# Optimization experiments

Hardware: AMD Instinct MI355X
Metric: run time of the kernel (lower is better)

Reference implementation:

```python
import jax, jax.numpy as jnp
import numpy as np

B, L, D = 2, 4096, 2048
H = 8
DK = D // H   # head qk dim = 256
DV = D // H   # head v dim = 256
KCONV = 4
BT = 64       # chunk size
EPS = 1e-5


def setup_inputs() -> dict:
    key = jax.random.key(0)
    ks = jax.random.split(key, 10)
    s = 0.02  # xavier-ish init scale (gain 2**-2.5)
    return {
        "hidden_states": jax.random.normal(ks[0], (B, L, D), jnp.float32),
        "Wq": jax.random.normal(ks[1], (D, D), jnp.float32) * s,
        "Wk": jax.random.normal(ks[2], (D, D), jnp.float32) * s,
        "Wv": jax.random.normal(ks[3], (D, D), jnp.float32) * s,
        "Wb": jax.random.normal(ks[4], (H, D), jnp.float32) * s,
        "conv_q": jax.random.normal(ks[5], (D, KCONV), jnp.float32) * 0.5,
        "conv_k": jax.random.normal(ks[6], (D, KCONV), jnp.float32) * 0.5,
        "conv_v": jax.random.normal(ks[7], (D, KCONV), jnp.float32) * 0.5,
        "g_norm": jnp.ones((DV,), jnp.float32),
        "Wo": jax.random.normal(ks[8], (D, D), jnp.float32) * s,
    }


def _causal_conv_silu(x, w):
    # depthwise causal conv1d (ShortConvolution), x: [B,L,C], w: [C,K]; silu activation
    K = w.shape[1]
    xp = jnp.pad(x, ((0, 0), (K - 1, 0), (0, 0)))
    Lx = x.shape[1]
    y = xp[:, 0:Lx, :] * w[:, 0]
    for j in range(1, K):
        y = y + xp[:, j:j + Lx, :] * w[:, j]
    return jax.nn.silu(y)


def _l2norm(x):
    return x * jax.lax.rsqrt(jnp.sum(x * x, -1, keepdims=True) + 1e-6)


def _chunk_delta_rule(q, k, v, beta):
    # q,k: [B,H,L,DK], v: [B,H,L,DV], beta: [B,H,L]
    b, h, Lq, dk = q.shape
    dv = v.shape[-1]
    nc = Lq // BT
    q = q * (dk ** -0.5)
    kb = k * beta[..., None]
    vb = v * beta[..., None]
    ch = lambda x: x.reshape(b, h, nc, BT, x.shape[-1])
    qc, kc, kbc, vbc = ch(q), ch(k), ch(kb), ch(vb)
    tri_s = jnp.tril(jnp.ones((BT, BT), bool), -1)  # strictly lower
    tri = jnp.tril(jnp.ones((BT, BT), bool))        # lower incl diag
    # M = strict_lower(K_beta K^T); T = (I+M)^{-1} via unit-lower triangular solve
    M = jnp.where(tri_s, jnp.einsum('bhntd,bhnsd->bhnts', kbc, kc), 0.0)
    Lmat = jnp.eye(BT, dtype=q.dtype) + M
    W = jax.scipy.linalg.solve_triangular(Lmat, kbc, lower=True, unit_diagonal=True)  # T @ k_beta
    U = jax.scipy.linalg.solve_triangular(Lmat, vbc, lower=True, unit_diagonal=True)  # T @ v_beta

    def step(S, xs):
        q_i, k_i, w_i, u_i = xs  # each [b,h,BT,d]
        attn = jnp.where(tri, jnp.einsum('bhtd,bhsd->bhts', q_i, k_i), 0.0)
        u_new = u_i - jnp.einsum('bhtd,bhdv->bhtv', w_i, S)
        o_i = jnp.einsum('bhtd,bhdv->bhtv', q_i, S) + jnp.einsum('bhts,bhsv->bhtv', attn, u_new)
        S = S + jnp.einsum('bhtd,bhtv->bhdv', k_i, u_new)
        return S, o_i

    mv = lambda x: jnp.moveaxis(x, 2, 0)  # chunk axis to front for scan
    S0 = jnp.zeros((b, h, dk, dv), q.dtype)
    S, o = jax.lax.scan(step, S0, (mv(qc), mv(kc), mv(W), mv(U)))
    o = jnp.moveaxis(o, 0, 2).reshape(b, h, Lq, dv)
    return o, S


def reference(hidden_states, Wq, Wk, Wv, Wb, conv_q, conv_k, conv_v, g_norm, Wo):
    hs = hidden_states
    q = _causal_conv_silu(hs @ Wq.T, conv_q)
    k = _causal_conv_silu(hs @ Wk.T, conv_k)
    v = _causal_conv_silu(hs @ Wv.T, conv_v)
    tohead = lambda x: x.reshape(B, L, H, -1).transpose(0, 2, 1, 3)  # b l (h d) -> b h l d
    q, k, v = tohead(q), tohead(k), tohead(v)
    q, k = _l2norm(q), _l2norm(k)
    beta = jax.nn.sigmoid(hs @ Wb.T).transpose(0, 2, 1)  # [B,H,L]
    o, _ = _chunk_delta_rule(q, k, v, beta)
    o = o.transpose(0, 2, 1, 3)  # [B,L,H,DV]
    o = o * jax.lax.rsqrt(jnp.mean(o * o, -1, keepdims=True) + EPS) * g_norm  # per-head RMSNorm
    return o.reshape(B, L, D) @ Wo.T
```

## Files before the change

### kernel.cpp

```cpp
#include <hip/hip_runtime.h>
#include <stdint.h>

#define TOK    8192
#define LDIM   4096
#define DDIM   2048
#define NBH    16
#define DK     256
#define NCHUNK 64
#define DVS    16

typedef __attribute__((ext_vector_type(8))) short bf16x8;
typedef __attribute__((ext_vector_type(4))) float f32x4;

#define MFMA(a,b,c) __builtin_amdgcn_mfma_f32_16x16x32_bf16((a),(b),(c),0,0,0)

__device__ __forceinline__ unsigned short f2bf(float f){
  union { float f; uint32_t u; } v; v.f = f;
  uint32_t r = v.u + 0x7FFFu + ((v.u >> 16) & 1u);
  return (unsigned short)(r >> 16);
}
__device__ __forceinline__ float bf2f(unsigned short u){
  union { uint32_t u; float f; } v; v.u = ((uint32_t)u) << 16;
  return v.f;
}

typedef __attribute__((address_space(1))) unsigned int as1_u32;
typedef __attribute__((address_space(3))) unsigned int as3_u32;
__device__ __forceinline__ void gload16(const void* g, void* l){
  __builtin_amdgcn_global_load_lds((const as1_u32*)g, (as3_u32*)l, 16, 0, 0);
}

__global__ void k_guard(float* o){ if (threadIdx.x == 0) o[0] = 0.f; }

__global__ __launch_bounds__(256) void k_f2bf(const float* __restrict__ s,
                                              unsigned short* __restrict__ d, int n)
{
  int i = (blockIdx.x*256 + threadIdx.x)*4;
  if (i >= n) return;
  float4 v = *(const float4*)(s + i);
  ushort4 o; o.x=f2bf(v.x); o.y=f2bf(v.y); o.z=f2bf(v.z); o.w=f2bf(v.w);
  *(ushort4*)(d + i) = o;
}

__global__ __launch_bounds__(256) void k_beta(const float* __restrict__ hs,
                                              const float* __restrict__ Wb,
                                              float* __restrict__ beta)
{
  const long t = blockIdx.x;
  const int tid = threadIdx.x;
  float acc[8] = {0,0,0,0,0,0,0,0};
  const float* xr = hs + t*DDIM;
  for (int i = tid; i < DDIM; i += 256){
    float x = xr[i];
    #pragma unroll
    for (int h=0; h<8; h++) acc[h] += x * Wb[h*DDIM + i];
  }
  __shared__ float red[8][4];
  const int w = tid >> 6, lane = tid & 63;
  #pragma unroll
  for (int h=0; h<8; h++){
    float s = acc[h];
    #pragma unroll
    for (int off=32; off; off>>=1) s += __shfl_down(s, off, 64);
    if (lane == 0) red[h][w] = s;
  }
  __syncthreads();
  if (tid < 8){
    float s = red[tid][0]+red[tid][1]+red[tid][2]+red[tid][3];
    float bv = 1.f/(1.f + __expf(-s));
    int b = (int)(t >> 12), l = (int)(t & 4095);
    beta[((long)(b*8 + tid))*LDIM + l] = bv;
  }
}

template <bool F32OUT>
__global__ __launch_bounds__(256,2) void k_gemm_bt(
    const unsigned short* __restrict__ A, const unsigned short* __restrict__ Bw,
    void* __restrict__ Cv, int M, int N, int K)
{
  __shared__ unsigned short As[128*32];
  __shared__ unsigned short Bs[128*32];
  const int tid = threadIdx.x;
  const int w = tid >> 6, l = tid & 63;
  const int lo = l & 15, quad = l >> 4;
  const int wm = w >> 1, wn = w & 1;
  const int gx = gridDim.x;
  int id = blockIdx.y * gx + blockIdx.x;
  const int nwg = gx * gridDim.y;
  if ((nwg & 7) == 0){
    const int q8 = nwg >> 3;
    id = (id & 7) * q8 + (id >> 3);
  }
  const int bx = id % gx, by = id / gx;
  const long tm = (long)by * 128, tn = (long)bx * 128;
  const int slot0 = (w*2+0)*64 + l;
  const int slot1 = (w*2+1)*64 + l;
  const int r0 = slot0 >> 2, c0 = (slot0 & 3) * 8;
  const int r1 = slot1 >> 2, c1 = (slot1 & 3) * 8;
  const unsigned short* pA0 = A  + (tm + r0)*(long)K + c0;
  const unsigned short* pA1 = A  + (tm + r1)*(long)K + c1;
  const unsigned short* pB0 = Bw + (tn + r0)*(long)K + c0;
  const unsigned short* pB1 = Bw + (tn + r1)*(long)K + c1;
  unsigned short* lA0 = &As[slot0*8]; unsigned short* lA1 = &As[slot1*8];
  unsigned short* lB0 = &Bs[slot0*8]; unsigned short* lB1 = &Bs[slot1*8];
  f32x4 acc[4][4] = {};
  for (int k0 = 0; k0 < K; k0 += 32){
    __syncthreads();
    gload16(pA0 + k0, lA0);
    gload16(pA1 + k0, lA1);
    gload16(pB0 + k0, lB0);
    gload16(pB1 + k0, lB1);
    __syncthreads();
    bf16x8 af[4], bg[4];
    #pragma unroll
    for (int i=0;i<4;i++){
      af[i] = *(const bf16x8*)&As[(wm*64 + i*16 + lo)*32 + quad*8];
      bg[i] = *(const bf16x8*)&Bs[(wn*64 + i*16 + lo)*32 + quad*8];
    }
    #pragma unroll
    for (int mt=0; mt<4; mt++)
      #pragma unroll
      for (int nt=0; nt<4; nt++)
        acc[mt][nt] = MFMA(af[mt], bg[nt], acc[mt][nt]);
  }
  #pragma unroll
  for (int mt=0; mt<4; mt++)
    #pragma unroll
    for (int nt=0; nt<4; nt++)
      #pragma unroll
      for (int r=0; r<4; r++){
        long m = tm + wm*64 + mt*16 + quad*4 + r;
        long n = tn + wn*64 + nt*16 + lo;
        if (F32OUT) ((float*)Cv)[m*N + n] = acc[mt][nt][r];
        else ((unsigned short*)Cv)[m*N + n] = f2bf(acc[mt][nt][r]);
      }
}

__global__ __launch_bounds__(256) void k_conv(
  const unsigned short* __restrict__ X, const float* __restrict__ Wc,
  const float* __restrict__ beta,
  unsigned short* __restrict__ O, int mode)
{
  const int lt = blockIdx.x, bh = blockIdx.y;
  const int b = bh >> 3, h = bh & 7;
  const int d = threadIdx.x;
  const int ch = h*256 + d;
  const int l0 = lt*64;
  const unsigned short* xp = X + (long)b*LDIM*DDIM + ch;
  const float4 wv = *(const float4*)(Wc + ch*4);
  float x0=0.f, x1=0.f, x2=0.f;
  if (l0 >= 3){
    x0 = bf2f(xp[(long)(l0-3)*DDIM]);
    x1 = bf2f(xp[(long)(l0-2)*DDIM]);
    x2 = bf2f(xp[(long)(l0-1)*DDIM]);
  }
  float y[64];
  #pragma unroll
  for (int i=0;i<64;i++){
    float x3 = bf2f(xp[(long)(l0+i)*DDIM]);
    float s = x0*wv.x + x1*wv.y + x2*wv.z + x3*wv.w;
    y[i] = s / (1.f + __expf(-s));
    x0 = x1; x1 = x2; x2 = x3;
  }
  unsigned short* op = O + (long)bh*LDIM*DK + d;
  if (mode == 2){
    const float* bet = beta + (long)bh*LDIM + l0;
    #pragma unroll
    for (int i=0;i<64;i++) op[(long)(l0+i)*DK] = f2bf(y[i]*bet[i]);
    return;
  }
  __shared__ float red[64*4];
  __shared__ float scl[64];
  const int wv_i = threadIdx.x >> 6, lane = threadIdx.x & 63;
  #pragma unroll
  for (int i=0;i<64;i++){
    float ss = y[i]*y[i];
    #pragma unroll
    for (int off=32; off; off>>=1) ss += __shfl_down(ss, off, 64);
    if (lane == 0) red[i*4 + wv_i] = ss;
  }
  __syncthreads();
  if (threadIdx.x < 64){
    int i = threadIdx.x;
    float s = red[i*4]+red[i*4+1]+red[i*4+2]+red[i*4+3];
    scl[i] = rsqrtf(s + 1e-6f) * (mode==0 ? 0.0625f : 1.f);
  }
  __syncthreads();
  #pragma unroll
  for (int i=0;i<64;i++) op[(long)(l0+i)*DK] = f2bf(y[i]*scl[i]);
}

__global__ __launch_bounds__(256) void k_transpose(
  const unsigned short* __restrict__ kH, unsigned short* __restrict__ kT)
{
  const int lt = blockIdx.x, dt = blockIdx.y, bh = blockIdx.z;
  __shared__ unsigned short tk[64][72];
  const int tid = threadIdx.x;
  const int rl = tid >> 2, c0 = (tid & 3) * 16;
  const long base = ((long)bh*LDIM + lt*64 + rl)*DK + dt*64 + c0;
  *(bf16x8*)&tk[rl][c0]   = *(const bf16x8*)(kH + base);
  *(bf16x8*)&tk[rl][c0+8] = *(const bf16x8*)(kH + base + 8);
  __syncthreads();
  const int rd = tid >> 2, lc0 = (tid & 3) * 16;
  bf16x8 ok0, ok1;
  #pragma unroll
  for (int j=0;j<16;j++){
    unsigned short kraw = tk[lc0+j][rd];
    if (j < 8) ok0[j] = (short)kraw; else ok1[j-8] = (short)kraw;
  }
  const long ob = (((long)bh*NCHUNK + lt)*DK + dt*64 + rd)*64 + lc0;
  *(bf16x8*)(kT + ob) = ok0; *(bf16x8*)(kT + ob + 8) = ok1;
}

__global__ __launch_bounds__(256) void k_passA(
  const unsigned short* __restrict__ qH, const unsigned short* __restrict__ kH,
  const unsigned short* vbH,
  const unsigned short* __restrict__ kT,
  const float* __restrict__ beta,
  unsigned short* Wout,
  unsigned short* __restrict__ Uout,
  unsigned short* __restrict__ Aout)
{
  const int c = blockIdx.x, bh = blockIdx.y;
  __shared__ unsigned short Nn[64*72];
  __shared__ unsigned short NT[64*72];
  __shared__ unsigned short Pb[64*72];
  __shared__ unsigned short vT[256*72];
  const int tid = threadIdx.x;
  const int w = tid >> 6, l = tid & 63, lo = l & 15, quad = l >> 4;
  const long tokBase = (long)bh*LDIM + c*64;
  const unsigned short* qrow = qH + tokBase*DK;
  const unsigned short* krow = kH + tokBase*DK;
  const float bv = beta[tokBase + w*16 + lo];

  {
    const int r = tid >> 2, cs = (tid & 3) * 64;
    const unsigned short* vrow = vbH + (tokBase + r)*DK + cs;
    bf16x8 vv[8];
    #pragma unroll
    for (int j=0;j<8;j++) vv[j] = *(const bf16x8*)(vrow + j*8);
    #pragma unroll
    for (int j=0;j<8;j++)
      #pragma unroll
      for (int e=0;e<8;e++)
        vT[(cs + j*8 + e)*72 + r] = (unsigned short)vv[j][e];
  }

  f32x4 mAcc[4] = {}; f32x4 aAcc[4] = {};
  #pragma unroll
  for (int ks=0; ks<8; ks++){
    bf16x8 kf[4];
    #pragma unroll
    for (int nt=0; nt<4; nt++)
      kf[nt] = *(const bf16x8*)&krow[(nt*16+lo)*DK + ks*32 + quad*8];
    bf16x8 qf  = *(const bf16x8*)&qrow[(w*16+lo)*DK + ks*32 + quad*8];
    bf16x8 kfw = *(const bf16x8*)&krow[(w*16+lo)*DK + ks*32 + quad*8];
    bf16x8 kbf;
    #pragma unroll
    for (int j=0;j<8;j++) kbf[j] = (short)f2bf(bf2f((unsigned short)kfw[j]) * bv);
    #pragma unroll
    for (int nt=0; nt<4; nt++){
      mAcc[nt] = MFMA(kbf, kf[nt], mAcc[nt]);
      aAcc[nt] = MFMA(qf,  kf[nt], aAcc[nt]);
    }
  }
  unsigned short* Ap = Aout + ((long)bh*NCHUNK + c)*64*64;
  #pragma unroll
  for (int nt=0; nt<4; nt++)
    #pragma unroll
    for (int r=0; r<4; r++){
      int t = w*16 + quad*4 + r, s = nt*16 + lo;
      float mv = (t > s) ? mAcc[nt][r] : 0.f;
      unsigned short mb = f2bf(mv);
      Nn[t*72+s] = mb;
      NT[s*72+t] = mb;
      Pb[t*72+s] = f2bf((t==s ? 1.f : 0.f) - mv);
      Ap[t*64+s] = f2bf((t >= s) ? aAcc[nt][r] : 0.f);
    }
  __syncthreads();

  #pragma unroll 1
  for (int it=0; it<5; it++){
    bf16x8 aN[2], aP[2], bN[2][4];
    #pragma unroll
    for (int ks=0; ks<2; ks++){
      aN[ks] = *(const bf16x8*)&Nn[(w*16+lo)*72 + ks*32 + quad*8];
      aP[ks] = *(const bf16x8*)&Pb[(w*16+lo)*72 + ks*32 + quad*8];
      #pragma unroll
      for (int nt=0; nt<4; nt++)
        bN[ks][nt] = *(const bf16x8*)&NT[(nt*16+lo)*72 + ks*32 + quad*8];
    }
    f32x4 pp[4];
    #pragma unroll
    for (int nt=0; nt<4; nt++)
      #pragma unroll
      for (int r=0; r<4; r++)
        pp[nt][r] = bf2f(Pb[(w*16+quad*4+r)*72 + nt*16+lo]);
    __syncthreads();
    f32x4 sq[4] = {};
    #pragma unroll
    for (int ks=0; ks<2; ks++)
      #pragma unroll
      for (int nt=0; nt<4; nt++)
        sq[nt] = MFMA(aN[ks], bN[ks][nt], sq[nt]);
    #pragma unroll
    for (int nt=0; nt<4; nt++)
      #pragma unroll
      for (int r=0; r<4; r++){
        int t = w*16 + quad*4 + r, s = nt*16 + lo;
        unsigned short vb2 = f2bf(sq[nt][r]);
        Nn[t*72+s] = vb2; NT[s*72+t] = vb2;
      }
    __syncthreads();
    #pragma unroll
    for (int ks=0; ks<2; ks++)
      #pragma unroll
      for (int nt=0; nt<4; nt++){
        bf16x8 b = *(const bf16x8*)&NT[(nt*16+lo)*72 + ks*32 + quad*8];
        pp[nt] = MFMA(aP[ks], b, pp[nt]);
      }
    #pragma unroll
    for (int nt=0; nt<4; nt++)
      #pragma unroll
      for (int r=0; r<4; r++)
        Pb[(w*16+quad*4+r)*72 + nt*16+lo] = f2bf(pp[nt][r]);
    __syncthreads();
  }

  float b8[2][8];
  #pragma unroll
  for (int ks=0; ks<2; ks++)
    #pragma unroll
    for (int e=0; e<8; e++)
      b8[ks][e] = beta[tokBase + ks*32 + quad*8 + e];
  const unsigned short* kTb = kT + ((long)bh*NCHUNK + c)*DK*64;
  unsigned short* Wp = Wout + tokBase*DK;
  unsigned short* Up = Uout + tokBase*DK;
  #pragma unroll 1
  for (int nl=0; nl<4; nl++){
    const int d = (w*4 + nl)*16 + lo;
    f32x4 wa[4] = {}; f32x4 ua[4] = {};
    #pragma unroll
    for (int ks=0; ks<2; ks++){
      bf16x8 braw = *(const bf16x8*)&kTb[(long)d*64 + ks*32 + quad*8];
      bf16x8 bw;
      #pragma unroll
      for (int e=0; e<8; e++) bw[e] = (short)f2bf(bf2f((unsigned short)braw[e]) * b8[ks][e]);
      bf16x8 bu = *(const bf16x8*)&vT[d*72 + ks*32 + quad*8];
      #pragma unroll
      for (int mt=0; mt<4; mt++){
        bf16x8 a = *(const bf16x8*)&Pb[(mt*16+lo)*72 + ks*32 + quad*8];
        wa[mt] = MFMA(a, bw, wa[mt]);
        ua[mt] = MFMA(a, bu, ua[mt]);
      }
    }
    #pragma unroll
    for (int mt=0; mt<4; mt++)
      #pragma unroll
      for (int r=0; r<4; r++){
        int t = mt*16 + quad*4 + r;
        Wp[t*DK + d] = f2bf(wa[mt][r]);
        Up[t*DK + d] = f2bf(ua[mt][r]);
      }
  }
}

__device__ __forceinline__ int sidx(int n, int d){
  return n*256 + (((d>>3) ^ (n&7))<<3) + (d&7);
}
__device__ __forceinline__ int uidx(int n, int t){
  return n*64 + ((((t>>3) ^ (n&7)) & 7)<<3) + (t&7);
}

struct PrefWU {
  bf16x8 wf[8];
  unsigned short uf[4];
};

__device__ __forceinline__ void load_wu(PrefWU& P,
    const unsigned short* __restrict__ Wp, const unsigned short* __restrict__ Up,
    int c, int w, int lo, int quad, int vb)
{
  const unsigned short* Wc = Wp + (long)c*64*DK;
  const unsigned short* Uc = Up + (long)c*64*DK;
  #pragma unroll
  for (int ks=0; ks<8; ks++)
    P.wf[ks] = *(const bf16x8*)&Wc[(w*16+lo)*DK + ks*32 + quad*8];
  const int t0 = w*16 + quad*4;
  #pragma unroll
  for (int r=0; r<4; r++)
    P.uf[r] = Uc[(t0+r)*DK + vb*DVS + lo];
}

__device__ __forceinline__ void scan_chunk(PrefWU& P, int c, int cnext,
  const unsigned short* __restrict__ Wp, const unsigned short* __restrict__ Up,
  const unsigned short* __restrict__ qp, const unsigned short* __restrict__ kTp,
  const unsigned short* __restrict__ Ap, unsigned short* __restrict__ op,
  const unsigned short* __restrict__ Srd, unsigned short* __restrict__ Swr,
  unsigned short* __restrict__ u_l, f32x4 (&S)[4],
  int w, int lo, int quad, int vb)
{
  const unsigned short* qc = qp + (long)c*64*DK;
  const unsigned short* Ac = Ap + (long)c*64*64;
  const unsigned short* kc = kTp + (long)c*DK*64;
  const int t0 = w*16 + quad*4;
  bf16x8 qf[8], af[2];
  #pragma unroll
  for (int ks=0; ks<8; ks++)
    qf[ks] = *(const bf16x8*)&qc[(w*16+lo)*DK + ks*32 + quad*8];
  #pragma unroll
  for (int ks=0; ks<2; ks++)
    af[ks] = *(const bf16x8*)&Ac[(w*16+lo)*64 + ks*32 + quad*8];

  bf16x8 sb[8];
  #pragma unroll
  for (int ks=0; ks<8; ks++)
    sb[ks] = *(const bf16x8*)&Srd[sidx(lo, ks*32+quad*8)];
  f32x4 ua0 = {}, ua1 = {};
  #pragma unroll
  for (int ks=0; ks<4; ks++){
    ua0 = MFMA(P.wf[ks],   sb[ks],   ua0);
    ua1 = MFMA(P.wf[ks+4], sb[ks+4], ua1);
  }
  {
    ushort4 pk;
    pk.x = f2bf(bf2f(P.uf[0]) - (ua0[0]+ua1[0]));
    pk.y = f2bf(bf2f(P.uf[1]) - (ua0[1]+ua1[1]));
    pk.z = f2bf(bf2f(P.uf[2]) - (ua0[2]+ua1[2]));
    pk.w = f2bf(bf2f(P.uf[3]) - (ua0[3]+ua1[3]));
    *(ushort4*)&u_l[uidx(lo, t0)] = pk;
  }
  __syncthreads();

  load_wu(P, Wp, Up, cnext, w, lo, quad, vb);
  bf16x8 kf[4][2];
  #pragma unroll
  for (int mtl=0; mtl<4; mtl++)
    #pragma unroll
    for (int ks=0; ks<2; ks++)
      kf[mtl][ks] = *(const bf16x8*)&kc[(w*64+mtl*16+lo)*64 + ks*32 + quad*8];

  f32x4 oa0 = {}, oa1 = {};
  #pragma unroll
  for (int ks=0; ks<4; ks++){
    oa0 = MFMA(qf[ks],   sb[ks],   oa0);
    oa1 = MFMA(qf[ks+4], sb[ks+4], oa1);
  }
  bf16x8 ub[2];
  #pragma unroll
  for (int ks=0; ks<2; ks++)
    ub[ks] = *(const bf16x8*)&u_l[uidx(lo, ks*32+quad*8)];
  #pragma unroll
  for (int ks=0; ks<2; ks++)
    oa0 = MFMA(af[ks], ub[ks], oa0);
  #pragma unroll
  for (int r=0; r<4; r++)
    op[(long)(c*64 + t0 + r)*DK + vb*DVS + lo] = f2bf(oa0[r] + oa1[r]);

  #pragma unroll
  for (int mtl=0; mtl<4; mtl++)
    #pragma unroll
    for (int ks=0; ks<2; ks++)
      S[mtl] = MFMA(kf[mtl][ks], ub[ks], S[mtl]);
  #pragma unroll
  for (int mtl=0; mtl<4; mtl++){
    const int d0 = w*64 + mtl*16 + quad*4;
    ushort4 pk;
    pk.x = f2bf(S[mtl][0]); pk.y = f2bf(S[mtl][1]);
    pk.z = f2bf(S[mtl][2]); pk.w = f2bf(S[mtl][3]);
    *(ushort4*)&Swr[sidx(lo, d0)] = pk;
  }
  __syncthreads();
}

__global__ __launch_bounds__(256,1) void k_scan(
  const unsigned short* __restrict__ Wm, const unsigned short* __restrict__ Um,
  const unsigned short* __restrict__ qH, const unsigned short* __restrict__ kT,
  const unsigned short* __restrict__ Abuf, unsigned short* __restrict__ oH)
{
  const int bh = blockIdx.x, vb = blockIdx.y;
  __shared__ unsigned short S_l[2][DVS*256];
  __shared__ unsigned short u_l[DVS*64];
  const int tid = threadIdx.x;
  const int w = tid >> 6, l = tid & 63, lo = l & 15, quad = l >> 4;
  for (int i = tid; i < DVS*256/4; i += 256) ((unsigned long long*)S_l[0])[i] = 0ULL;
  f32x4 S[4] = {};
  const long hb = (long)bh * LDIM;
  const unsigned short* Wp = Wm + hb*DK;
  const unsigned short* Up = Um + hb*DK;
  const unsigned short* qp = qH + hb*DK;
  const unsigned short* kTp = kT + (long)bh*NCHUNK*DK*64;
  const unsigned short* Ap = Abuf + (long)bh*NCHUNK*64*64;
  unsigned short* op = oH + hb*DK;
  PrefWU P;
  load_wu(P, Wp, Up, 0, w, lo, quad, vb);
  __syncthreads();
  #pragma unroll 1
  for (int c = 0; c < NCHUNK; c += 2){
    scan_chunk(P, c,   c+1, Wp, Up, qp, kTp, Ap, op, S_l[0], S_l[1], u_l, S, w, lo, quad, vb);
    scan_chunk(P, c+1, (c+2 < NCHUNK) ? c+2 : NCHUNK-1,
               Wp, Up, qp, kTp, Ap, op, S_l[1], S_l[0], u_l, S, w, lo, quad, vb);
  }
}

__global__ __launch_bounds__(64) void k_rms(
  const unsigned short* __restrict__ oH, const float* __restrict__ g,
  unsigned short* __restrict__ oN)
{
  const int ln = blockIdx.x, bh = blockIdx.y;
  const int b = bh >> 3, h = bh & 7;
  ushort4 u = *(const ushort4*)(oH + ((long)bh*LDIM + ln)*DK + threadIdx.x*4);
  float4 v; v.x = bf2f(u.x); v.y = bf2f(u.y); v.z = bf2f(u.z); v.w = bf2f(u.w);
  float ss = v.x*v.x + v.y*v.y + v.z*v.z + v.w*v.w;
  #pragma unroll
  for (int off=32; off; off>>=1) ss += __shfl_down(ss, off, 64);
  ss = __shfl(ss, 0, 64);
  const float sc = rsqrtf(ss*(1.f/DK) + 1e-5f);
  const float4 gv = *(const float4*)(g + threadIdx.x*4);
  unsigned short* o = oN + ((long)b*LDIM + ln)*DDIM + h*DK + threadIdx.x*4;
  ushort4 pk; pk.x=f2bf(v.x*sc*gv.x); pk.y=f2bf(v.y*sc*gv.y);
  pk.z=f2bf(v.z*sc*gv.z); pk.w=f2bf(v.w*sc*gv.w);
  *(ushort4*)o = pk;
}

extern "C" void kernel_launch(void* const* d_in, const int* in_sizes, int n_in,
                              void* d_out, int out_size, void* d_ws, size_t ws_size,
                              hipStream_t stream)
{
  (void)in_sizes; (void)n_in; (void)out_size;
  const float* hs = (const float*)d_in[0];
  const float* Wq = (const float*)d_in[1];
  const float* Wk = (const float*)d_in[2];
  const float* Wv = (const float*)d_in[3];
  const float* Wb = (const float*)d_in[4];
  const float* cq = (const float*)d_in[5];
  const float* ck = (const float*)d_in[6];
  const float* cv = (const float*)d_in[7];
  const float* gn = (const float*)d_in[8];
  const float* Wo = (const float*)d_in[9];

  const size_t SZ_TD2 = (size_t)TOK*DDIM*2;
  const size_t SZ_DD2 = (size_t)DDIM*DDIM*2;
  const size_t NEED  = 5*SZ_TD2 + 2*SZ_DD2 + (size_t)NBH*LDIM*4;
  const size_t NEEDW = NEED + SZ_TD2;
  if (ws_size < NEED){ k_guard<<<1, 64, 0, stream>>>((float*)d_out); return; }

  char* p = (char*)d_ws;
  unsigned short* bufA = (unsigned short*)p;      p += SZ_TD2;
  unsigned short* bufB = (unsigned short*)p;      p += SZ_DD2;
  unsigned short* bufC = (unsigned short*)p;      p += SZ_TD2;
  unsigned short* bufD = (unsigned short*)p;      p += SZ_TD2;
  unsigned short* bufE = (unsigned short*)p;      p += SZ_TD2;
  unsigned short* bufF = (unsigned short*)p;      p += SZ_TD2;
  unsigned short* bufG = (unsigned short*)p;      p += SZ_DD2;
  float*          beta = (float*)p;               p += (size_t)NBH*LDIM*4;
  unsigned short* bufW = (ws_size >= NEEDW) ? (unsigned short*)p : bufF;

  const dim3 gg(DDIM/128, TOK/128);
  const dim3 cg(LDIM/64, NBH);
  const int nTD = TOK*DDIM, nDD = DDIM*DDIM;

  k_f2bf<<<dim3(nTD/1024), 256, 0, stream>>>(hs, bufA, nTD);
  k_beta<<<dim3(TOK), 256, 0, stream>>>(hs, Wb, beta);

  k_f2bf<<<dim3(nDD/1024), 256, 0, stream>>>(Wq, bufB, nDD);
  k_gemm_bt<false><<<gg, 256, 0, stream>>>(bufA, bufB, bufC, TOK, DDIM, DDIM);
  k_conv<<<cg, 256, 0, stream>>>(bufC, cq, beta, bufD, 0);

  k_f2bf<<<dim3(nDD/1024), 256, 0, stream>>>(Wk, bufB, nDD);
  k_gemm_bt<false><<<gg, 256, 0, stream>>>(bufA, bufB, bufC, TOK, DDIM, DDIM);
  k_conv<<<cg, 256, 0, stream>>>(bufC, ck, beta, bufE, 1);

  k_f2bf<<<dim3(nDD/1024), 256, 0, stream>>>(Wv, bufB, nDD);
  k_gemm_bt<false><<<gg, 256, 0, stream>>>(bufA, bufB, bufC, TOK, DDIM, DDIM);
  k_conv<<<cg, 256, 0, stream>>>(bufC, cv, beta, bufF, 2);

  k_transpose<<<dim3(LDIM/64, DK/64, NBH), 256, 0, stream>>>(bufE, bufC);
  k_passA<<<dim3(NCHUNK, NBH), 256, 0, stream>>>(bufD, bufE, bufF, bufC, beta,
                                                 bufW, bufA , bufG);
  k_scan<<<dim3(NBH, 16), 256, 0, stream>>>(bufW, bufA, bufD, bufC, bufG, bufE);
  k_rms<<<dim3(LDIM, NBH), 64, 0, stream>>>(bufE, gn, bufC);

  k_f2bf<<<dim3(nDD/1024), 256, 0, stream>>>(Wo, bufB, nDD);
  k_gemm_bt<true><<<gg, 256, 0, stream>>>(bufC, bufB, d_out , TOK, DDIM, DDIM);
}
```

Baseline: 912.6 us.

## Run scan with one wavefront per block, dropping barriers and double-buffered state

```diff
diff --git a/kernel.cpp b/kernel.cpp
--- a/kernel.cpp
+++ b/kernel.cpp
@@ -372,134 +372,102 @@
   return n*64 + ((((t>>3) ^ (n&7)) & 7)<<3) + (t&7);
 }
 
-struct PrefWU {
-  bf16x8 wf[8];
-  unsigned short uf[4];
-};
-
-__device__ __forceinline__ void load_wu(PrefWU& P,
-    const unsigned short* __restrict__ Wp, const unsigned short* __restrict__ Up,
-    int c, int w, int lo, int quad, int vb)
-{
-  const unsigned short* Wc = Wp + (long)c*64*DK;
-  const unsigned short* Uc = Up + (long)c*64*DK;
-  #pragma unroll
-  for (int ks=0; ks<8; ks++)
-    P.wf[ks] = *(const bf16x8*)&Wc[(w*16+lo)*DK + ks*32 + quad*8];
-  const int t0 = w*16 + quad*4;
-  #pragma unroll
-  for (int r=0; r<4; r++)
-    P.uf[r] = Uc[(t0+r)*DK + vb*DVS + lo];
-}
-
-__device__ __forceinline__ void scan_chunk(PrefWU& P, int c, int cnext,
-  const unsigned short* __restrict__ Wp, const unsigned short* __restrict__ Up,
-  const unsigned short* __restrict__ qp, const unsigned short* __restrict__ kTp,
-  const unsigned short* __restrict__ Ap, unsigned short* __restrict__ op,
-  const unsigned short* __restrict__ Srd, unsigned short* __restrict__ Swr,
-  unsigned short* __restrict__ u_l, f32x4 (&S)[4],
-  int w, int lo, int quad, int vb)
-{
-  const unsigned short* qc = qp + (long)c*64*DK;
-  const unsigned short* Ac = Ap + (long)c*64*64;
-  const unsigned short* kc = kTp + (long)c*DK*64;
-  const int t0 = w*16 + quad*4;
-  bf16x8 qf[8], af[2];
-  #pragma unroll
-  for (int ks=0; ks<8; ks++)
-    qf[ks] = *(const bf16x8*)&qc[(w*16+lo)*DK + ks*32 + quad*8];
-  #pragma unroll
-  for (int ks=0; ks<2; ks++)
-    af[ks] = *(const bf16x8*)&Ac[(w*16+lo)*64 + ks*32 + quad*8];
-
-  bf16x8 sb[8];
-  #pragma unroll
-  for (int ks=0; ks<8; ks++)
-    sb[ks] = *(const bf16x8*)&Srd[sidx(lo, ks*32+quad*8)];
-  f32x4 ua0 = {}, ua1 = {};
-  #pragma unroll
-  for (int ks=0; ks<4; ks++){
-    ua0 = MFMA(P.wf[ks],   sb[ks],   ua0);
-    ua1 = MFMA(P.wf[ks+4], sb[ks+4], ua1);
-  }
-  {
-    ushort4 pk;
-    pk.x = f2bf(bf2f(P.uf[0]) - (ua0[0]+ua1[0]));
-    pk.y = f2bf(bf2f(P.uf[1]) - (ua0[1]+ua1[1]));
-    pk.z = f2bf(bf2f(P.uf[2]) - (ua0[2]+ua1[2]));
-    pk.w = f2bf(bf2f(P.uf[3]) - (ua0[3]+ua1[3]));
-    *(ushort4*)&u_l[uidx(lo, t0)] = pk;
-  }
-  __syncthreads();
-
-  load_wu(P, Wp, Up, cnext, w, lo, quad, vb);
-  bf16x8 kf[4][2];
-  #pragma unroll
-  for (int mtl=0; mtl<4; mtl++)
-    #pragma unroll
-    for (int ks=0; ks<2; ks++)
-      kf[mtl][ks] = *(const bf16x8*)&kc[(w*64+mtl*16+lo)*64 + ks*32 + quad*8];
-
-  f32x4 oa0 = {}, oa1 = {};
-  #pragma unroll
-  for (int ks=0; ks<4; ks++){
-    oa0 = MFMA(qf[ks],   sb[ks],   oa0);
-    oa1 = MFMA(qf[ks+4], sb[ks+4], oa1);
-  }
-  bf16x8 ub[2];
-  #pragma unroll
-  for (int ks=0; ks<2; ks++)
-    ub[ks] = *(const bf16x8*)&u_l[uidx(lo, ks*32+quad*8)];
-  #pragma unroll
-  for (int ks=0; ks<2; ks++)
-    oa0 = MFMA(af[ks], ub[ks], oa0);
-  #pragma unroll
-  for (int r=0; r<4; r++)
-    op[(long)(c*64 + t0 + r)*DK + vb*DVS + lo] = f2bf(oa0[r] + oa1[r]);
-
-  #pragma unroll
-  for (int mtl=0; mtl<4; mtl++)
-    #pragma unroll
-    for (int ks=0; ks<2; ks++)
-      S[mtl] = MFMA(kf[mtl][ks], ub[ks], S[mtl]);
-  #pragma unroll
-  for (int mtl=0; mtl<4; mtl++){
-    const int d0 = w*64 + mtl*16 + quad*4;
-    ushort4 pk;
-    pk.x = f2bf(S[mtl][0]); pk.y = f2bf(S[mtl][1]);
-    pk.z = f2bf(S[mtl][2]); pk.w = f2bf(S[mtl][3]);
-    *(ushort4*)&Swr[sidx(lo, d0)] = pk;
-  }
-  __syncthreads();
-}
-
-__global__ __launch_bounds__(256,1) void k_scan(
+__global__ __launch_bounds__(64,1) void k_scan(
   const unsigned short* __restrict__ Wm, const unsigned short* __restrict__ Um,
   const unsigned short* __restrict__ qH, const unsigned short* __restrict__ kT,
   const unsigned short* __restrict__ Abuf, unsigned short* __restrict__ oH)
 {
   const int bh = blockIdx.x, vb = blockIdx.y;
-  __shared__ unsigned short S_l[2][DVS*256];
+  __shared__ unsigned short S_l[DVS*256];
   __shared__ unsigned short u_l[DVS*64];
-  const int tid = threadIdx.x;
-  const int w = tid >> 6, l = tid & 63, lo = l & 15, quad = l >> 4;
-  for (int i = tid; i < DVS*256/4; i += 256) ((unsigned long long*)S_l[0])[i] = 0ULL;
-  f32x4 S[4] = {};
+  const int l = threadIdx.x & 63, lo = l & 15, quad = l >> 4;
+  for (int i = l; i < DVS*256/4; i += 64) ((unsigned long long*)S_l)[i] = 0ULL;
+  f32x4 S[16] = {};
   const long hb = (long)bh * LDIM;
-  const unsigned short* Wp = Wm + hb*DK;
-  const unsigned short* Up = Um + hb*DK;
-  const unsigned short* qp = qH + hb*DK;
+  const unsigned short* Wp  = Wm + hb*DK;
+  const unsigned short* Up  = Um + hb*DK;
+  const unsigned short* qp  = qH + hb*DK;
   const unsigned short* kTp = kT + (long)bh*NCHUNK*DK*64;
-  const unsigned short* Ap = Abuf + (long)bh*NCHUNK*64*64;
+  const unsigned short* Ap  = Abuf + (long)bh*NCHUNK*64*64;
   unsigned short* op = oH + hb*DK;
-  PrefWU P;
-  load_wu(P, Wp, Up, 0, w, lo, quad, vb);
-  __syncthreads();
+
   #pragma unroll 1
-  for (int c = 0; c < NCHUNK; c += 2){
-    scan_chunk(P, c,   c+1, Wp, Up, qp, kTp, Ap, op, S_l[0], S_l[1], u_l, S, w, lo, quad, vb);
-    scan_chunk(P, c+1, (c+2 < NCHUNK) ? c+2 : NCHUNK-1,
-               Wp, Up, qp, kTp, Ap, op, S_l[1], S_l[0], u_l, S, w, lo, quad, vb);
+  for (int c = 0; c < NCHUNK; ++c){
+    const unsigned short* Wc = Wp + (long)c*64*DK;
+    const unsigned short* Uc = Up + (long)c*64*DK;
+    const unsigned short* qc = qp + (long)c*64*DK;
+    const unsigned short* Ac = Ap + (long)c*64*64;
+    const unsigned short* kc = kTp + (long)c*DK*64;
+
+    bf16x8 sb[8];
+    #pragma unroll
+    for (int ks=0; ks<8; ks++)
+      sb[ks] = *(const bf16x8*)&S_l[sidx(lo, ks*32+quad*8)];
+
+    #pragma unroll
+    for (int mt=0; mt<4; mt++){
+      bf16x8 wf[8];
+      #pragma unroll
+      for (int ks=0; ks<8; ks++)
+        wf[ks] = *(const bf16x8*)&Wc[(mt*16+lo)*DK + ks*32 + quad*8];
+      unsigned short uf[4];
+      #pragma unroll
+      for (int r=0; r<4; r++)
+        uf[r] = Uc[(mt*16+quad*4+r)*DK + vb*DVS + lo];
+      f32x4 a0 = {}, a1 = {};
+      #pragma unroll
+      for (int ks=0; ks<4; ks++){
+        a0 = MFMA(wf[ks],   sb[ks],   a0);
+        a1 = MFMA(wf[ks+4], sb[ks+4], a1);
+      }
+      ushort4 pk;
+      pk.x = f2bf(bf2f(uf[0]) - (a0[0]+a1[0]));
+      pk.y = f2bf(bf2f(uf[1]) - (a0[1]+a1[1]));
+      pk.z = f2bf(bf2f(uf[2]) - (a0[2]+a1[2]));
+      pk.w = f2bf(bf2f(uf[3]) - (a0[3]+a1[3]));
+      *(ushort4*)&u_l[uidx(lo, mt*16+quad*4)] = pk;
+    }
+
+    bf16x8 ub[2];
+    #pragma unroll
+    for (int ks=0; ks<2; ks++)
+      ub[ks] = *(const bf16x8*)&u_l[uidx(lo, ks*32+quad*8)];
+
+    #pragma unroll
+    for (int mt=0; mt<4; mt++){
+      bf16x8 qf[8], af[2];
+      #pragma unroll
+      for (int ks=0; ks<8; ks++)
+        qf[ks] = *(const bf16x8*)&qc[(mt*16+lo)*DK + ks*32 + quad*8];
+      #pragma unroll
+      for (int ks=0; ks<2; ks++)
+        af[ks] = *(const bf16x8*)&Ac[(mt*16+lo)*64 + ks*32 + quad*8];
+      f32x4 o0 = {}, o1 = {};
+      #pragma unroll
+      for (int ks=0; ks<4; ks++){
+        o0 = MFMA(qf[ks],   sb[ks],   o0);
+        o1 = MFMA(qf[ks+4], sb[ks+4], o1);
+      }
+      #pragma unroll
+      for (int ks=0; ks<2; ks++)
+        o0 = MFMA(af[ks], ub[ks], o0);
+      #pragma unroll
+      for (int r=0; r<4; r++)
+        op[(long)(c*64 + mt*16 + quad*4 + r)*DK + vb*DVS + lo] = f2bf(o0[r] + o1[r]);
+    }
+
+    #pragma unroll
+    for (int mtl=0; mtl<16; mtl++){
+      bf16x8 k0 = *(const bf16x8*)&kc[(mtl*16+lo)*64 + 0*32 + quad*8];
+      bf16x8 k1 = *(const bf16x8*)&kc[(mtl*16+lo)*64 + 1*32 + quad*8];
+      S[mtl] = MFMA(k0, ub[0], S[mtl]);
+      S[mtl] = MFMA(k1, ub[1], S[mtl]);
+      const int d0 = mtl*16 + quad*4;
+      ushort4 pk;
+      pk.x = f2bf(S[mtl][0]); pk.y = f2bf(S[mtl][1]);
+      pk.z = f2bf(S[mtl][2]); pk.w = f2bf(S[mtl][3]);
+      *(ushort4*)&S_l[sidx(lo, d0)] = pk;
+    }
   }
 }
 
@@ -578,7 +546,7 @@
   k_transpose<<<dim3(LDIM/64, DK/64, NBH), 256, 0, stream>>>(bufE, bufC);
   k_passA<<<dim3(NCHUNK, NBH), 256, 0, stream>>>(bufD, bufE, bufF, bufC, beta,
                                                  bufW, bufA , bufG);
-  k_scan<<<dim3(NBH, 16), 256, 0, stream>>>(bufW, bufA, bufD, bufC, bufG, bufE);
+  k_scan<<<dim3(NBH, 16), 64, 0, stream>>>(bufW, bufA, bufD, bufC, bufG, bufE);
   k_rms<<<dim3(LDIM, NBH), 64, 0, stream>>>(bufE, gn, bufC);
 
   k_f2bf<<<dim3(nDD/1024), 256, 0, stream>>>(Wo, bufB, nDD);
```

Measured after the change: 1.752 ms. 91.9% more time.

## Replace GEMM with 256x256-tile, 4-stage pipelined, LDS-swizzled kernel

Applied to the files above, without the earlier changes.

```diff
diff --git a/kernel.cpp b/kernel.cpp
--- a/kernel.cpp
+++ b/kernel.cpp
@@ -30,6 +30,10 @@
   __builtin_amdgcn_global_load_lds((const as1_u32*)g, (as3_u32*)l, 16, 0, 0);
 }
 
+__device__ __forceinline__ void bar_lds(){
+  asm volatile("s_waitcnt lgkmcnt(0)\n\ts_barrier" ::: "memory");
+}
+
 __global__ void k_guard(float* o){ if (threadIdx.x == 0) o[0] = 0.f; }
 
 __global__ __launch_bounds__(256) void k_f2bf(const float* __restrict__ s,
@@ -74,65 +78,83 @@
 }
 
 template <bool F32OUT>
-__global__ __launch_bounds__(256,2) void k_gemm_bt(
+__global__ __launch_bounds__(512) void k_gemm256(
     const unsigned short* __restrict__ A, const unsigned short* __restrict__ Bw,
     void* __restrict__ Cv, int M, int N, int K)
 {
-  __shared__ unsigned short As[128*32];
-  __shared__ unsigned short Bs[128*32];
+  __shared__ unsigned short As[4][256*32];
+  __shared__ unsigned short Bs[4][256*32];
   const int tid = threadIdx.x;
   const int w = tid >> 6, l = tid & 63;
   const int lo = l & 15, quad = l >> 4;
-  const int wm = w >> 1, wn = w & 1;
+  const int wm = w >> 2, wn = w & 3;
   const int gx = gridDim.x;
   int id = blockIdx.y * gx + blockIdx.x;
   const int nwg = gx * gridDim.y;
-  if ((nwg & 7) == 0){
-    const int q8 = nwg >> 3;
-    id = (id & 7) * q8 + (id >> 3);
-  }
+  if ((nwg & 7) == 0){ const int q8 = nwg >> 3; id = (id & 7)*q8 + (id >> 3); }
   const int bx = id % gx, by = id / gx;
-  const long tm = (long)by * 128, tn = (long)bx * 128;
+  const long tm = (long)by * 256, tn = (long)bx * 256;
+
   const int slot0 = (w*2+0)*64 + l;
   const int slot1 = (w*2+1)*64 + l;
-  const int r0 = slot0 >> 2, c0 = (slot0 & 3) * 8;
-  const int r1 = slot1 >> 2, c1 = (slot1 & 3) * 8;
-  const unsigned short* pA0 = A  + (tm + r0)*(long)K + c0;
-  const unsigned short* pA1 = A  + (tm + r1)*(long)K + c1;
-  const unsigned short* pB0 = Bw + (tn + r0)*(long)K + c0;
-  const unsigned short* pB1 = Bw + (tn + r1)*(long)K + c1;
-  unsigned short* lA0 = &As[slot0*8]; unsigned short* lA1 = &As[slot1*8];
-  unsigned short* lB0 = &Bs[slot0*8]; unsigned short* lB1 = &Bs[slot1*8];
-  f32x4 acc[4][4] = {};
-  for (int k0 = 0; k0 < K; k0 += 32){
-    __syncthreads();
-    gload16(pA0 + k0, lA0);
-    gload16(pA1 + k0, lA1);
-    gload16(pB0 + k0, lB0);
-    gload16(pB1 + k0, lB1);
-    __syncthreads();
-    bf16x8 af[4], bg[4];
-    #pragma unroll
-    for (int i=0;i<4;i++){
-      af[i] = *(const bf16x8*)&As[(wm*64 + i*16 + lo)*32 + quad*8];
-      bg[i] = *(const bf16x8*)&Bs[(wn*64 + i*16 + lo)*32 + quad*8];
-    }
-    #pragma unroll
-    for (int mt=0; mt<4; mt++)
-      #pragma unroll
-      for (int nt=0; nt<4; nt++)
-        acc[mt][nt] = MFMA(af[mt], bg[nt], acc[mt][nt]);
-  }
-  #pragma unroll
-  for (int mt=0; mt<4; mt++)
-    #pragma unroll
-    for (int nt=0; nt<4; nt++)
+  const int r0 = slot0 >> 2, c0 = ((slot0 & 3)*16) ^ ((r0 & 3) << 4);
+  const int r1 = slot1 >> 2, c1 = ((slot1 & 3)*16) ^ ((r1 & 3) << 4);
+  const unsigned short* pA0 = A  + (tm + r0)*(long)K + (c0 >> 1);
+  const unsigned short* pA1 = A  + (tm + r1)*(long)K + (c1 >> 1);
+  const unsigned short* pB0 = Bw + (tn + r0)*(long)K + (c0 >> 1);
+  const unsigned short* pB1 = Bw + (tn + r1)*(long)K + (c1 >> 1);
+  const int asw = ((quad*16) ^ ((lo & 3) << 4)) >> 1;
+
+  f32x4 acc[8][4] = {};
+  const int nt = K >> 5;
+
+#define STAGE(t_) do { const int kk_ = (t_)*32, b_ = (t_) & 3;      \
+    gload16(pA0 + kk_, &As[b_][slot0*8]);                           \
+    gload16(pA1 + kk_, &As[b_][slot1*8]);                           \
+    gload16(pB0 + kk_, &Bs[b_][slot0*8]);                           \
+    gload16(pB1 + kk_, &Bs[b_][slot1*8]); } while(0)
+
+#define COMPUTE(t_) do { const int b_ = (t_) & 3;                              \
+    bf16x8 af[8], bg[4];                                                       \
+    _Pragma("unroll")                                                          \
+    for (int mf=0; mf<8; mf++)                                                 \
+      af[mf] = *(const bf16x8*)&As[b_][(wm*128 + mf*16 + lo)*32 + asw];        \
+    _Pragma("unroll")                                                          \
+    for (int nf=0; nf<4; nf++)                                                 \
+      bg[nf] = *(const bf16x8*)&Bs[b_][(wn*64 + nf*16 + lo)*32 + asw];         \
+    _Pragma("unroll")                                                          \
+    for (int mf=0; mf<8; mf++)                                                 \
+      _Pragma("unroll")                                                        \
+      for (int nf=0; nf<4; nf++)                                               \
+        acc[mf][nf] = MFMA(af[mf], bg[nf], acc[mf][nf]); } while(0)
+
+  STAGE(0); STAGE(1);
+  #pragma unroll 1
+  for (int t = 0; t < nt-2; ++t){
+    STAGE(t+2);
+    asm volatile("s_waitcnt vmcnt(8)" ::: "memory");
+    bar_lds();
+    COMPUTE(t);
+  }
+  asm volatile("s_waitcnt vmcnt(4)" ::: "memory");
+  bar_lds();
+  COMPUTE(nt-2);
+  asm volatile("s_waitcnt vmcnt(0)" ::: "memory");
+  bar_lds();
+  COMPUTE(nt-1);
+#undef STAGE
+#undef COMPUTE
+
+  #pragma unroll
+  for (int mf=0; mf<8; mf++)
+    #pragma unroll
+    for (int nf=0; nf<4; nf++)
       #pragma unroll
       for (int r=0; r<4; r++){
-        long m = tm + wm*64 + mt*16 + quad*4 + r;
-        long n = tn + wn*64 + nt*16 + lo;
-        if (F32OUT) ((float*)Cv)[m*N + n] = acc[mt][nt][r];
-        else ((unsigned short*)Cv)[m*N + n] = f2bf(acc[mt][nt][r]);
+        long m = tm + wm*128 + mf*16 + quad*4 + r;
+        long n = tn + wn*64 + nf*16 + lo;
+        if (F32OUT) ((float*)Cv)[m*N + n] = acc[mf][nf][r];
+        else ((unsigned short*)Cv)[m*N + n] = f2bf(acc[mf][nf][r]);
       }
 }
 
@@ -556,7 +578,7 @@
   float*          beta = (float*)p;               p += (size_t)NBH*LDIM*4;
   unsigned short* bufW = (ws_size >= NEEDW) ? (unsigned short*)p : bufF;
 
-  const dim3 gg(DDIM/128, TOK/128);
+  const dim3 gg(DDIM/256, TOK/256);
   const dim3 cg(LDIM/64, NBH);
   const int nTD = TOK*DDIM, nDD = DDIM*DDIM;
 
@@ -564,15 +586,15 @@
   k_beta<<<dim3(TOK), 256, 0, stream>>>(hs, Wb, beta);
 
   k_f2bf<<<dim3(nDD/1024), 256, 0, stream>>>(Wq, bufB, nDD);
-  k_gemm_bt<false><<<gg, 256, 0, stream>>>(bufA, bufB, bufC, TOK, DDIM, DDIM);
+  k_gemm256<false><<<gg, 512, 0, stream>>>(bufA, bufB, bufC, TOK, DDIM, DDIM);
   k_conv<<<cg, 256, 0, stream>>>(bufC, cq, beta, bufD, 0);
 
   k_f2bf<<<dim3(nDD/1024), 256, 0, stream>>>(Wk, bufB, nDD);
-  k_gemm_bt<false><<<gg, 256, 0, stream>>>(bufA, bufB, bufC, TOK, DDIM, DDIM);
+  k_gemm256<false><<<gg, 512, 0, stream>>>(bufA, bufB, bufC, TOK, DDIM, DDIM);
   k_conv<<<cg, 256, 0, stream>>>(bufC, ck, beta, bufE, 1);
 
   k_f2bf<<<dim3(nDD/1024), 256, 0, stream>>>(Wv, bufB, nDD);
-  k_gemm_bt<false><<<gg, 256, 0, stream>>>(bufA, bufB, bufC, TOK, DDIM, DDIM);
+  k_gemm256<false><<<gg, 512, 0, stream>>>(bufA, bufB, bufC, TOK, DDIM, DDIM);
   k_conv<<<cg, 256, 0, stream>>>(bufC, cv, beta, bufF, 2);
 
   k_transpose<<<dim3(LDIM/64, DK/64, NBH), 256, 0, stream>>>(bufE, bufC);
@@ -582,5 +604,5 @@
   k_rms<<<dim3(LDIM, NBH), 64, 0, stream>>>(bufE, gn, bufC);
 
   k_f2bf<<<dim3(nDD/1024), 256, 0, stream>>>(Wo, bufB, nDD);
-  k_gemm_bt<true><<<gg, 256, 0, stream>>>(bufC, bufB, d_out , TOK, DDIM, DDIM);
-}
+  k_gemm256<true><<<gg, 512, 0, stream>>>(bufC, bufB, d_out , TOK, DDIM, DDIM);
+}
```

Measured after the change: 868.4 us. 1.05x faster.
